# Optimization experiments

Hardware: AMD Instinct MI355X
Metric: run time of the kernel (lower is better)

The kernel has to match this reference:

```python
import jax, jax.numpy as jnp
import numpy as np

N_PER_G = 18
GRAPHS = 4096
N = GRAPHS * N_PER_G            # 73728 nodes
E = GRAPHS * N_PER_G * (N_PER_G - 1)  # 1253376 edges (fully connected per graph)
F_IN = 1536                     # sfreq * timestep
EPS = 1e-5
SLOPE = 0.01


def _lrelu(v):
    return jnp.where(v >= 0, v, SLOPE * v)


def setup_inputs() -> dict:
    key = jax.random.key(0)
    ks = jax.random.split(key, 32)
    # node features
    x = jax.random.normal(ks[0], (N, F_IN), dtype=jnp.float32)
    # fully-connected edges within each 18-node graph
    src, dst = np.meshgrid(np.arange(N_PER_G), np.arange(N_PER_G), indexing='ij')
    m = src != dst
    src, dst = src[m], dst[m]                      # [306]
    offs = (np.arange(GRAPHS) * N_PER_G)[:, None]
    row = (offs + src[None, :]).reshape(-1)
    col = (offs + dst[None, :]).reshape(-1)
    edge_index = jnp.asarray(np.stack([row, col]), dtype=jnp.int32)  # [2,E]
    edge_weight = jax.random.uniform(ks[1], (E,), dtype=jnp.float32)
    batch = jnp.asarray(np.arange(N) // N_PER_G, dtype=jnp.int32)

    def lin(k, fi, fo):
        kw, kb = jax.random.split(k)
        s = 1.0 / np.sqrt(fi)
        W = jax.random.uniform(kw, (fi, fo), jnp.float32, -s, s)
        b = jax.random.uniform(kb, (fo,), jnp.float32, -s, s)
        return W, b

    def bn(k, f):
        k1, k2 = jax.random.split(k)
        g = jnp.ones((f,), jnp.float32)
        be = jnp.zeros((f,), jnp.float32)
        rm = jax.random.normal(k1, (f,), jnp.float32) * 0.1
        rv = jax.random.uniform(k2, (f,), jnp.float32) + 0.5
        return g, be, rm, rv

    W1, b1 = lin(ks[2], F_IN, 32)
    W2, b2 = lin(ks[3], 32, 64)
    W3, b3 = lin(ks[4], 64, 128)
    g1, be1, rm1, rv1 = bn(ks[5], 32)
    g2, be2, rm2, rv2 = bn(ks[6], 64)
    g3, be3, rm3, rv3 = bn(ks[7], 128)
    fW1, fb1 = lin(ks[8], 128, 64)
    fW2, fb2 = lin(ks[9], 64, 32)
    fW3, fb3 = lin(ks[10], 32, 16)
    fW4, fb4 = lin(ks[11], 16, 1)

    return dict(x=x, edge_index=edge_index, edge_weight=edge_weight, batch=batch,
                W1=W1, b1=b1, g1=g1, be1=be1, rm1=rm1, rv1=rv1,
                W2=W2, b2=b2, g2=g2, be2=be2, rm2=rm2, rv2=rv2,
                W3=W3, b3=b3, g3=g3, be3=be3, rm3=rm3, rv3=rv3,
                fW1=fW1, fb1=fb1, fW2=fW2, fb2=fb2,
                fW3=fW3, fb3=fb3, fW4=fW4, fb4=fb4)


def _gcn_norm(edge_index, edge_weight):
    # add self loops (weight 1), symmetric normalization (PyG GCNConv, improved=False)
    row = jnp.concatenate([edge_index[0], jnp.arange(N, dtype=edge_index.dtype)])
    col = jnp.concatenate([edge_index[1], jnp.arange(N, dtype=edge_index.dtype)])
    w = jnp.concatenate([edge_weight, jnp.ones((N,), edge_weight.dtype)])
    deg = jax.ops.segment_sum(w, col, num_segments=N)
    dinv = jnp.where(deg > 0, jax.lax.rsqrt(jnp.maximum(deg, 1e-30)), 0.0)
    norm = dinv[row] * w * dinv[col]
    return row, col, norm


def _gcn(x, W, b, row, col, norm):
    h = x @ W                                       # [N, Fout]
    out = jax.ops.segment_sum(norm[:, None] * h[row], col, num_segments=N)
    return out + b


def _bn(h, g, be, rm, rv):
    return (h - rm) * jax.lax.rsqrt(rv + EPS) * g + be


def reference(x, edge_index, edge_weight, batch,
              W1, b1, g1, be1, rm1, rv1,
              W2, b2, g2, be2, rm2, rv2,
              W3, b3, g3, be3, rm3, rv3,
              fW1, fb1, fW2, fb2, fW3, fb3, fW4, fb4):
    row, col, norm = _gcn_norm(edge_index, edge_weight)
    h = _lrelu(_bn(_gcn(x, W1, b1, row, col, norm), g1, be1, rm1, rv1))
    h = _lrelu(_bn(_gcn(h, W2, b2, row, col, norm), g2, be2, rm2, rv2))
    h = _lrelu(_bn(_gcn(h, W3, b3, row, col, norm), g3, be3, rm3, rv3))
    # global mean pool over graphs
    sums = jax.ops.segment_sum(h, batch, num_segments=GRAPHS)
    cnt = jax.ops.segment_sum(jnp.ones((N,), h.dtype), batch, num_segments=GRAPHS)
    h = sums / jnp.maximum(cnt, 1.0)[:, None]       # [G,128]
    # MLP head (dropout = identity in eval)
    h = _lrelu(h @ fW1 + fb1)
    h = _lrelu(h @ fW2 + fb2)
    h = _lrelu(h @ fW3 + fb3)
    h = h @ fW4 + fb4
    return h.squeeze(-1)                            # [G]
```

## Files before the change

### kernel.cpp

```cpp
#include <hip/hip_runtime.h>
#include <stdint.h>

#define GRAPHS 4096
#define NPG 18
#define EPERG 306
#define FIN 1536
#define BN_EPS 1e-5f
#define SLOPE 0.01f

using short8  = __attribute__((ext_vector_type(8))) short;
using ushort8 = __attribute__((ext_vector_type(8))) unsigned short;
using f32x4   = __attribute__((ext_vector_type(4))) float;

__device__ __forceinline__ unsigned short f2bf(float f) {
  unsigned u = __builtin_bit_cast(unsigned, f);
  u += 0x7fffu + ((u >> 16) & 1u);
  return (unsigned short)(u >> 16);
}

__global__ void prep_kernel(const float* __restrict__ W1,
    const float* __restrict__ b1, const float* __restrict__ g1,
    const float* __restrict__ be1, const float* __restrict__ rm1, const float* __restrict__ rv1,
    const float* __restrict__ b2, const float* __restrict__ g2,
    const float* __restrict__ be2, const float* __restrict__ rm2, const float* __restrict__ rv2,
    const float* __restrict__ b3, const float* __restrict__ g3,
    const float* __restrict__ be3, const float* __restrict__ rm3, const float* __restrict__ rv3,
    const float* __restrict__ W2, const float* __restrict__ W3,
    const float* __restrict__ fW1,
    unsigned short* __restrict__ w1frag, float* __restrict__ ab,
    float* __restrict__ W2t, float* __restrict__ W3t, float* __restrict__ fW1t) {
  const int tid = threadIdx.x;
  if (blockIdx.x < 24) {
    int slot = blockIdx.x * 256 + tid;
    int L  = slot & 63;
    int nt = (slot >> 6) & 1;
    int ks = slot >> 7;
    int n  = nt * 16 + (L & 15);
    int kb = ks * 32 + ((L >> 4) << 3);
    ushort8 v;
#pragma unroll
    for (int j = 0; j < 8; ++j) v[j] = f2bf(W1[(kb + j) * 32 + n]);
    *((ushort8*)w1frag + slot) = v;
  } else if (blockIdx.x == 24) {
    if (tid < 32) {
      float a = g1[tid] * rsqrtf(rv1[tid] + BN_EPS);
      ab[tid] = a; ab[32 + tid] = (b1[tid] - rm1[tid]) * a + be1[tid];
    }
    if (tid < 64) {
      float a = g2[tid] * rsqrtf(rv2[tid] + BN_EPS);
      ab[64 + tid] = a; ab[128 + tid] = (b2[tid] - rm2[tid]) * a + be2[tid];
    }
    if (tid < 128) {
      float a = g3[tid] * rsqrtf(rv3[tid] + BN_EPS);
      ab[192 + tid] = a; ab[320 + tid] = (b3[tid] - rm3[tid]) * a + be3[tid];
    }
  } else if (blockIdx.x == 25) {
    for (int i = tid; i < 64 * 32; i += 256) {
      int cc = i >> 5, k = i & 31;
      W2t[i] = W2[k * 64 + cc];
    }
  } else if (blockIdx.x == 26) {
    for (int i = tid; i < 128 * 64; i += 256) {
      int cc = i >> 6, k = i & 63;
      W3t[i] = W3[k * 128 + cc];
    }
  } else {
    for (int i = tid; i < 64 * 128; i += 256) {
      int cc = i >> 7, k = i & 127;
      fW1t[i] = fW1[k * 64 + cc];
    }
  }
}

__global__ __launch_bounds__(128, 4) void l1_gemm(
    const float* __restrict__ x, const unsigned short* __restrict__ w1frag,
    float* __restrict__ p1) {
  const int lane = threadIdx.x & 63;
  const int wv   = threadIdx.x >> 6;
  const int mt   = blockIdx.x * 2 + wv;
  const int row  = mt * 16 + (lane & 15);
  const float* __restrict__ xr = x + (size_t)row * FIN + ((lane >> 4) << 3);
  const short8* __restrict__ wf = (const short8*)w1frag + lane;

  f32x4 acc0 = {0.f, 0.f, 0.f, 0.f};
  f32x4 acc1 = {0.f, 0.f, 0.f, 0.f};

#pragma unroll 4
  for (int ks = 0; ks < 48; ++ks) {
    float4 a0 = *(const float4*)(xr + ks * 32);
    float4 a1 = *(const float4*)(xr + ks * 32 + 4);
    short8 af;
    af[0] = (short)f2bf(a0.x); af[1] = (short)f2bf(a0.y);
    af[2] = (short)f2bf(a0.z); af[3] = (short)f2bf(a0.w);
    af[4] = (short)f2bf(a1.x); af[5] = (short)f2bf(a1.y);
    af[6] = (short)f2bf(a1.z); af[7] = (short)f2bf(a1.w);
    short8 b0 = wf[(ks * 2 + 0) * 64];
    short8 b1 = wf[(ks * 2 + 1) * 64];
    acc0 = __builtin_amdgcn_mfma_f32_16x16x32_bf16(af, b0, acc0, 0, 0, 0);
    acc1 = __builtin_amdgcn_mfma_f32_16x16x32_bf16(af, b1, acc1, 0, 0, 0);
  }

  const int crow = mt * 16 + ((lane >> 4) << 2);
  const int ccol = lane & 15;
  float* p = p1 + (size_t)crow * 32 + ccol;
#pragma unroll
  for (int q = 0; q < 4; ++q) {
    p[q * 32]      = acc0[q];
    p[q * 32 + 16] = acc1[q];
  }
}

__global__ __launch_bounds__(256, 4) void gcn_rest(
    const float* __restrict__ ew, const float* __restrict__ p1,
    const float* __restrict__ W2t, const float* __restrict__ W3t,
    const float* __restrict__ fW1t, const float* __restrict__ fb1,
    const float* __restrict__ fW2, const float* __restrict__ fb2,
    const float* __restrict__ fW3, const float* __restrict__ fb3,
    const float* __restrict__ fW4, const float* __restrict__ fb4,
    const float* __restrict__ ab, float* __restrict__ out) {
  const int g   = blockIdx.x;
  const int tid = threadIdx.x;

  __shared__ float ew_s[EPERG];
  __shared__ float dinv_s[NPG];
  __shared__ float An[NPG][NPG + 1];
  __shared__ __align__(16) float Pb[NPG][132];
  __shared__ __align__(16) float Hb[NPG][132];
  __shared__ __align__(16) float pooled[128];
  __shared__ float m1[64];
  __shared__ float m2[32];
  __shared__ float m3[16];

  for (int i = tid; i < EPERG; i += 256) ew_s[i] = ew[g * EPERG + i];
  for (int i = tid; i < NPG * 32; i += 256) Pb[i >> 5][i & 31] = p1[g * 576 + i];
  __syncthreads();

  if (tid < NPG) {
    float deg = 1.0f;
#pragma unroll
    for (int j = 0; j < 17; ++j) {
      int s = j + (j >= tid);
      deg += ew_s[s * 17 + (tid - (tid > s ? 1 : 0))];
    }
    dinv_s[tid] = rsqrtf(deg);
  }
  __syncthreads();

  for (int o = tid; o < NPG * NPG; o += 256) {
    int d = o / NPG, s = o - d * NPG;
    float v;
    if (d == s) v = dinv_s[d] * dinv_s[d];
    else        v = dinv_s[s] * ew_s[s * 17 + (d - (d > s ? 1 : 0))] * dinv_s[d];
    An[d][s] = v;
  }
  __syncthreads();

  for (int o = tid; o < NPG * 32; o += 256) {
    int d = o >> 5, cc = o & 31;
    float s = 0.f;
#pragma unroll
    for (int ss = 0; ss < NPG; ++ss) s = fmaf(An[d][ss], Pb[ss][cc], s);
    float v = fmaf(s, ab[cc], ab[32 + cc]);
    Hb[d][cc] = v >= 0.f ? v : SLOPE * v;
  }
  __syncthreads();

  for (int o = tid; o < NPG * 32; o += 256) {
    int d = o >> 5, cc = o & 31;
    float s = 0.f;
#pragma unroll
    for (int ss = 0; ss < NPG; ++ss) s = fmaf(An[d][ss], Hb[ss][cc], s);
    Pb[d][cc] = s;
  }
  __syncthreads();

  for (int o = tid; o < NPG * 64; o += 256) {
    int r = o >> 6, cc = o & 63;
    const float4* gp = (const float4*)(&Pb[r][0]);
    const float4* wp = (const float4*)(W2t + cc * 32);
    float s = 0.f;
#pragma unroll
    for (int k4 = 0; k4 < 8; ++k4) {
      float4 a = gp[k4], b = wp[k4];
      s = fmaf(a.x, b.x, s); s = fmaf(a.y, b.y, s);
      s = fmaf(a.z, b.z, s); s = fmaf(a.w, b.w, s);
    }
    float v = fmaf(s, ab[64 + cc], ab[128 + cc]);
    Hb[r][cc] = v >= 0.f ? v : SLOPE * v;
  }
  __syncthreads();

  for (int o = tid; o < NPG * 64; o += 256) {
    int d = o >> 6, cc = o & 63;
    float s = 0.f;
#pragma unroll
    for (int ss = 0; ss < NPG; ++ss) s = fmaf(An[d][ss], Hb[ss][cc], s);
    Pb[d][cc] = s;
  }
  __syncthreads();

  for (int o = tid; o < NPG * 128; o += 256) {
    int r = o >> 7, cc = o & 127;
    const float4* gp = (const float4*)(&Pb[r][0]);
    const float4* wp = (const float4*)(W3t + cc * 64);
    float s = 0.f;
#pragma unroll
    for (int k4 = 0; k4 < 16; ++k4) {
      float4 a = gp[k4], b = wp[k4];
      s = fmaf(a.x, b.x, s); s = fmaf(a.y, b.y, s);
      s = fmaf(a.z, b.z, s); s = fmaf(a.w, b.w, s);
    }
    float v = fmaf(s, ab[192 + cc], ab[320 + cc]);
    Hb[r][cc] = v >= 0.f ? v : SLOPE * v;
  }
  __syncthreads();

  if (tid < 128) {
    float s = 0.f;
#pragma unroll
    for (int d = 0; d < NPG; ++d) s += Hb[d][tid];
    pooled[tid] = s * (1.0f / 18.0f);
  }
  __syncthreads();
  if (tid < 64) {
    const float4* pp = (const float4*)pooled;
    const float4* wp = (const float4*)(fW1t + tid * 128);
    float s = fb1[tid];
#pragma unroll
    for (int k4 = 0; k4 < 32; ++k4) {
      float4 a = pp[k4], b = wp[k4];
      s = fmaf(a.x, b.x, s); s = fmaf(a.y, b.y, s);
      s = fmaf(a.z, b.z, s); s = fmaf(a.w, b.w, s);
    }
    m1[tid] = s >= 0.f ? s : SLOPE * s;
  }
  __syncthreads();
  if (tid < 32) {
    float s = fb2[tid];
#pragma unroll
    for (int k = 0; k < 64; ++k) s = fmaf(m1[k], fW2[k * 32 + tid], s);
    m2[tid] = s >= 0.f ? s : SLOPE * s;
  }
  __syncthreads();
  if (tid < 16) {
    float s = fb3[tid];
#pragma unroll
    for (int k = 0; k < 32; ++k) s = fmaf(m2[k], fW3[k * 16 + tid], s);
    m3[tid] = s >= 0.f ? s : SLOPE * s;
  }
  __syncthreads();
  if (tid == 0) {
    float s = fb4[0];
#pragma unroll
    for (int k = 0; k < 16; ++k) s = fmaf(m3[k], fW4[k], s);
    out[g] = s;
  }
}

extern "C" void kernel_launch(void* const* d_in, const int* in_sizes, int n_in,
                              void* d_out, int out_size, void* d_ws, size_t ws_size,
                              hipStream_t stream) {
  const float* x   = (const float*)d_in[0];
  const float* ew  = (const float*)d_in[2];
  const float* W1  = (const float*)d_in[4];
  const float* b1  = (const float*)d_in[5];
  const float* g1  = (const float*)d_in[6];
  const float* be1 = (const float*)d_in[7];
  const float* rm1 = (const float*)d_in[8];
  const float* rv1 = (const float*)d_in[9];
  const float* W2  = (const float*)d_in[10];
  const float* b2  = (const float*)d_in[11];
  const float* g2  = (const float*)d_in[12];
  const float* be2 = (const float*)d_in[13];
  const float* rm2 = (const float*)d_in[14];
  const float* rv2 = (const float*)d_in[15];
  const float* W3  = (const float*)d_in[16];
  const float* b3  = (const float*)d_in[17];
  const float* g3  = (const float*)d_in[18];
  const float* be3 = (const float*)d_in[19];
  const float* rm3 = (const float*)d_in[20];
  const float* rv3 = (const float*)d_in[21];
  const float* fW1 = (const float*)d_in[22];
  const float* fb1 = (const float*)d_in[23];
  const float* fW2 = (const float*)d_in[24];
  const float* fb2 = (const float*)d_in[25];
  const float* fW3 = (const float*)d_in[26];
  const float* fb3 = (const float*)d_in[27];
  const float* fW4 = (const float*)d_in[28];
  const float* fb4 = (const float*)d_in[29];

  unsigned short* w1frag = (unsigned short*)d_ws;
  float* ab   = (float*)((char*)d_ws + 98304);
  float* W2t  = (float*)((char*)d_ws + 100352);
  float* W3t  = (float*)((char*)d_ws + 108544);
  float* fW1t = (float*)((char*)d_ws + 141312);
  float* p1   = (float*)((char*)d_ws + 174080);

  prep_kernel<<<28, 256, 0, stream>>>(W1, b1, g1, be1, rm1, rv1,
                                      b2, g2, be2, rm2, rv2,
                                      b3, g3, be3, rm3, rv3,
                                      W2, W3, fW1,
                                      w1frag, ab, W2t, W3t, fW1t);
  l1_gemm<<<2304, 128, 0, stream>>>(x, w1frag, p1);
  gcn_rest<<<GRAPHS, 256, 0, stream>>>(ew, p1, W2t, W3t, fW1t, fb1, fW2, fb2,
                                       fW3, fb3, fW4, fb4, ab, (float*)d_out);
}
```

Baseline: 747.0 us.

## Fuse layer-1 GEMM into per-graph GCN kernel using 32x32x16 MFMA split-K

Removes the separate l1_gemm kernel and its p1 intermediate buffer. Each per-graph block now computes the 18x32 projection of its own x rows: the four waves each take a quarter of K with a 32x32x16 bf16 MFMA, and the partial sums are reduced through shared memory. The W1 fragment layout in prep is changed to match the new MFMA shape. This saves one launch and the p1 round trip to global memory, but pads 18 rows up to 32 (44% of MFMA lanes wasted) and ties the x stream to a block that also does all the later layers.

After: 726.2 us. 2.8% less time.

```diff
diff --git a/kernel.cpp b/kernel.cpp
--- a/kernel.cpp
+++ b/kernel.cpp
@@ -11,6 +11,7 @@
 using short8  = __attribute__((ext_vector_type(8))) short;
 using ushort8 = __attribute__((ext_vector_type(8))) unsigned short;
 using f32x4   = __attribute__((ext_vector_type(4))) float;
+using f32x16  = __attribute__((ext_vector_type(16))) float;
 
 __device__ __forceinline__ unsigned short f2bf(float f) {
   unsigned u = __builtin_bit_cast(unsigned, f);
@@ -33,10 +34,9 @@
   if (blockIdx.x < 24) {
     int slot = blockIdx.x * 256 + tid;
     int L  = slot & 63;
-    int nt = (slot >> 6) & 1;
-    int ks = slot >> 7;
-    int n  = nt * 16 + (L & 15);
-    int kb = ks * 32 + ((L >> 4) << 3);
+    int ks = slot >> 6;
+    int n  = L & 31;
+    int kb = ks * 16 + ((L >> 5) << 3);
     ushort8 v;
 #pragma unroll
     for (int j = 0; j < 8; ++j) v[j] = f2bf(W1[(kb + j) * 32 + n]);
@@ -72,54 +72,19 @@
   }
 }
 
-__global__ __launch_bounds__(128, 4) void l1_gemm(
-    const float* __restrict__ x, const unsigned short* __restrict__ w1frag,
-    float* __restrict__ p1) {
-  const int lane = threadIdx.x & 63;
-  const int wv   = threadIdx.x >> 6;
-  const int mt   = blockIdx.x * 2 + wv;
-  const int row  = mt * 16 + (lane & 15);
-  const float* __restrict__ xr = x + (size_t)row * FIN + ((lane >> 4) << 3);
-  const short8* __restrict__ wf = (const short8*)w1frag + lane;
-
-  f32x4 acc0 = {0.f, 0.f, 0.f, 0.f};
-  f32x4 acc1 = {0.f, 0.f, 0.f, 0.f};
-
-#pragma unroll 4
-  for (int ks = 0; ks < 48; ++ks) {
-    float4 a0 = *(const float4*)(xr + ks * 32);
-    float4 a1 = *(const float4*)(xr + ks * 32 + 4);
-    short8 af;
-    af[0] = (short)f2bf(a0.x); af[1] = (short)f2bf(a0.y);
-    af[2] = (short)f2bf(a0.z); af[3] = (short)f2bf(a0.w);
-    af[4] = (short)f2bf(a1.x); af[5] = (short)f2bf(a1.y);
-    af[6] = (short)f2bf(a1.z); af[7] = (short)f2bf(a1.w);
-    short8 b0 = wf[(ks * 2 + 0) * 64];
-    short8 b1 = wf[(ks * 2 + 1) * 64];
-    acc0 = __builtin_amdgcn_mfma_f32_16x16x32_bf16(af, b0, acc0, 0, 0, 0);
-    acc1 = __builtin_amdgcn_mfma_f32_16x16x32_bf16(af, b1, acc1, 0, 0, 0);
-  }
-
-  const int crow = mt * 16 + ((lane >> 4) << 2);
-  const int ccol = lane & 15;
-  float* p = p1 + (size_t)crow * 32 + ccol;
-#pragma unroll
-  for (int q = 0; q < 4; ++q) {
-    p[q * 32]      = acc0[q];
-    p[q * 32 + 16] = acc1[q];
-  }
-}
-
-__global__ __launch_bounds__(256, 4) void gcn_rest(
-    const float* __restrict__ ew, const float* __restrict__ p1,
+__global__ __launch_bounds__(256, 4) void gcn_fused(
+    const float* __restrict__ x, const float* __restrict__ ew,
+    const unsigned short* __restrict__ w1frag, const float* __restrict__ ab,
     const float* __restrict__ W2t, const float* __restrict__ W3t,
     const float* __restrict__ fW1t, const float* __restrict__ fb1,
     const float* __restrict__ fW2, const float* __restrict__ fb2,
     const float* __restrict__ fW3, const float* __restrict__ fb3,
     const float* __restrict__ fW4, const float* __restrict__ fb4,
-    const float* __restrict__ ab, float* __restrict__ out) {
-  const int g   = blockIdx.x;
-  const int tid = threadIdx.x;
+    float* __restrict__ out) {
+  const int g    = blockIdx.x;
+  const int tid  = threadIdx.x;
+  const int lane = tid & 63;
+  const int wv   = tid >> 6;
 
   __shared__ float ew_s[EPERG];
   __shared__ float dinv_s[NPG];
@@ -132,7 +97,41 @@
   __shared__ float m3[16];
 
   for (int i = tid; i < EPERG; i += 256) ew_s[i] = ew[g * EPERG + i];
-  for (int i = tid; i < NPG * 32; i += 256) Pb[i >> 5][i & 31] = p1[g * 576 + i];
+
+  const int r  = lane & 31;
+  const int kg = lane >> 5;
+  const bool valid = (r < NPG);
+  f32x16 acc;
+#pragma unroll
+  for (int q = 0; q < 16; ++q) acc[q] = 0.f;
+
+  const float* __restrict__ xr =
+      x + (size_t)g * NPG * FIN + (size_t)r * FIN + (kg << 3);
+  const short8* __restrict__ wf = (const short8*)w1frag + lane;
+
+#pragma unroll 2
+  for (int ks = 0; ks < 24; ++ks) {
+    const int kidx = wv * 24 + ks;
+    float4 a0 = {0.f, 0.f, 0.f, 0.f}, a1 = {0.f, 0.f, 0.f, 0.f};
+    if (valid) {
+      a0 = *(const float4*)(xr + kidx * 16);
+      a1 = *(const float4*)(xr + kidx * 16 + 4);
+    }
+    short8 af;
+    af[0] = (short)f2bf(a0.x); af[1] = (short)f2bf(a0.y);
+    af[2] = (short)f2bf(a0.z); af[3] = (short)f2bf(a0.w);
+    af[4] = (short)f2bf(a1.x); af[5] = (short)f2bf(a1.y);
+    af[6] = (short)f2bf(a1.z); af[7] = (short)f2bf(a1.w);
+    short8 bf = wf[(size_t)kidx * 64];
+    acc = __builtin_amdgcn_mfma_f32_32x32x16_bf16(af, bf, acc, 0, 0, 0);
+  }
+
+  float* HbF = &Hb[0][0];
+#pragma unroll
+  for (int q = 0; q < 16; ++q) {
+    int rr = (q & 3) + ((q >> 2) << 3) + (kg << 2);
+    if (rr < NPG) HbF[wv * 576 + rr * 32 + r] = acc[q];
+  }
   __syncthreads();
 
   if (tid < NPG) {
@@ -143,6 +142,9 @@
       deg += ew_s[s * 17 + (tid - (tid > s ? 1 : 0))];
     }
     dinv_s[tid] = rsqrtf(deg);
+  }
+  for (int o = tid; o < NPG * 32; o += 256) {
+    Pb[o >> 5][o & 31] = HbF[o] + HbF[576 + o] + HbF[1152 + o] + HbF[1728 + o];
   }
   __syncthreads();
 
@@ -175,8 +177,8 @@
   __syncthreads();
 
   for (int o = tid; o < NPG * 64; o += 256) {
-    int r = o >> 6, cc = o & 63;
-    const float4* gp = (const float4*)(&Pb[r][0]);
+    int rrow = o >> 6, cc = o & 63;
+    const float4* gp = (const float4*)(&Pb[rrow][0]);
     const float4* wp = (const float4*)(W2t + cc * 32);
     float s = 0.f;
 #pragma unroll
@@ -186,7 +188,7 @@
       s = fmaf(a.z, b.z, s); s = fmaf(a.w, b.w, s);
     }
     float v = fmaf(s, ab[64 + cc], ab[128 + cc]);
-    Hb[r][cc] = v >= 0.f ? v : SLOPE * v;
+    Hb[rrow][cc] = v >= 0.f ? v : SLOPE * v;
   }
   __syncthreads();
 
@@ -200,8 +202,8 @@
   __syncthreads();
 
   for (int o = tid; o < NPG * 128; o += 256) {
-    int r = o >> 7, cc = o & 127;
-    const float4* gp = (const float4*)(&Pb[r][0]);
+    int rrow = o >> 7, cc = o & 127;
+    const float4* gp = (const float4*)(&Pb[rrow][0]);
     const float4* wp = (const float4*)(W3t + cc * 64);
     float s = 0.f;
 #pragma unroll
@@ -211,7 +213,7 @@
       s = fmaf(a.z, b.z, s); s = fmaf(a.w, b.w, s);
     }
     float v = fmaf(s, ab[192 + cc], ab[320 + cc]);
-    Hb[r][cc] = v >= 0.f ? v : SLOPE * v;
+    Hb[rrow][cc] = v >= 0.f ? v : SLOPE * v;
   }
   __syncthreads();
 
@@ -294,14 +296,13 @@
   float* W2t  = (float*)((char*)d_ws + 100352);
   float* W3t  = (float*)((char*)d_ws + 108544);
   float* fW1t = (float*)((char*)d_ws + 141312);
-  float* p1   = (float*)((char*)d_ws + 174080);
 
   prep_kernel<<<28, 256, 0, stream>>>(W1, b1, g1, be1, rm1, rv1,
                                       b2, g2, be2, rm2, rv2,
                                       b3, g3, be3, rm3, rv3,
                                       W2, W3, fW1,
                                       w1frag, ab, W2t, W3t, fW1t);
-  l1_gemm<<<2304, 128, 0, stream>>>(x, w1frag, p1);
-  gcn_rest<<<GRAPHS, 256, 0, stream>>>(ew, p1, W2t, W3t, fW1t, fb1, fW2, fb2,
-                                       fW3, fb3, fW4, fb4, ab, (float*)d_out);
+  gcn_fused<<<GRAPHS, 256, 0, stream>>>(x, ew, w1frag, ab, W2t, W3t, fW1t,
+                                        fb1, fW2, fb2, fW3, fb3, fW4, fb4,
+                                        (float*)d_out);
 }
```
